# Performance work log

Measured on AMD Instinct MI355X. Metric: run time of the kernel, lower is better.

Reference implementation:

```python
import jax, jax.numpy as jnp
import numpy as np

N_NODES = 100000
N_EDGES = 1000000
NHID = 128
N_CLASSES = 5000


def setup_inputs() -> dict:
    key = jax.random.key(0)
    ks = jax.random.split(key, 8)
    feature = jax.random.normal(ks[0], (N_NODES, NHID), dtype=jnp.float32)
    # Linear weights stored as [in, out] so forward is x @ W + b
    W1 = jax.random.normal(ks[1], (2 * NHID, NHID), dtype=jnp.float32) * (1.0 / np.sqrt(2 * NHID))
    b1 = jnp.zeros((NHID,), dtype=jnp.float32)
    alpha = jnp.full((NHID,), 0.25, dtype=jnp.float32)  # PReLU per-channel init
    W2 = jax.random.normal(ks[2], (NHID, 2), dtype=jnp.float32) * (1.0 / np.sqrt(NHID))
    b2 = jnp.zeros((2,), dtype=jnp.float32)
    row = jax.random.randint(ks[3], (N_EDGES,), 0, N_NODES, dtype=jnp.int64)
    col = jax.random.randint(ks[4], (N_EDGES,), 0, N_NODES, dtype=jnp.int64)
    label = jax.random.randint(ks[5], (N_NODES,), 0, N_CLASSES, dtype=jnp.int64)
    return {"feature": feature, "W1": W1, "b1": b1, "alpha": alpha,
            "W2": W2, "b2": b2, "row": row, "col": col, "label": label}


def reference(feature, W1, b1, alpha, W2, b2, row, col, label):
    # per-edge label: 1 if endpoints share a cluster label
    y = (label[row] == label[col]).astype(jnp.int32)  # [E]
    # edge gather + concat: [E, 2*nhid]
    x = jnp.concatenate([feature[row], feature[col]], axis=1)
    h = x @ W1 + b1                                   # [E, nhid]
    h = jnp.where(h >= 0, h, alpha * h)               # PReLU, per-channel alpha
    logits = h @ W2 + b2                              # [E, 2]
    logp = jax.nn.log_softmax(logits, axis=-1)
    # mean cross-entropy over edges
    loss = -jnp.mean(jnp.take_along_axis(logp, y[:, None], axis=1))
    return loss
```

## Files before the change

kernel.cpp:

```cpp
#include <hip/hip_runtime.h>
#include <hip/hip_bf16.h>

typedef __bf16 bf16_t;
typedef bf16_t bf16x8 __attribute__((ext_vector_type(8)));
typedef float floatx4 __attribute__((ext_vector_type(4)));
typedef float floatx2 __attribute__((ext_vector_type(2)));

#define N_NODES 100000
#define N_EDGES 1000000


__global__ __launch_bounds__(256) void k_prep(const float* __restrict__ W1,
                                              const float* __restrict__ b1,
                                              const float* __restrict__ alpha,
                                              const float* __restrict__ W2,
                                              const float* __restrict__ b2,
                                              bf16_t* __restrict__ WT,
                                              float* __restrict__ wabsp,
                                              float* __restrict__ w1g,
                                              float* __restrict__ constg,
                                              float* __restrict__ out) {
    const int t = threadIdx.x;
    if (blockIdx.x < 128) {
        int i = blockIdx.x * 256 + t;
        int n = i >> 7, k = i & 127;
        float v = (n < 128) ? W1[k * 128 + n] : W1[(k + 128) * 128 + (n - 128)];
        WT[i] = (bf16_t)v;
        return;
    }
    __shared__ float w1L[128];
    if (t < 128) {
        float wd = W2[2 * t + 1] - W2[2 * t];
        float al = alpha[t];
        float w1v = wd * (1.f + al) * 0.5f;
        w1L[t] = w1v;
        w1g[t] = w1v;
        int col = (t & 64) + (t & 3) * 16 + ((t >> 2) & 15);
        float wdc = W2[2 * col + 1] - W2[2 * col];
        wabsp[t] = wdc * (1.f - alpha[col]) * 0.5f;
    }
    __syncthreads();
    if (t < 64) {
        float c = fmaf(w1L[t], b1[t], w1L[t + 64] * b1[t + 64]);
#pragma unroll
        for (int m = 32; m >= 1; m >>= 1) c += __shfl_xor(c, m, 64);
        if (t == 0) { *constg = c + (b2[1] - b2[0]); out[0] = 0.f; }
    }
}

__device__ inline unsigned fp4_code(float x) {
    float a = fabsf(x);
    unsigned code = (unsigned)(a > 0.25f) + (a > 0.75f) + (a > 1.25f) + (a > 1.75f)
                  + (a > 2.5f) + (a > 3.5f) + (a > 5.0f);
    return code | (x < 0.f ? 8u : 0u);
}

__global__ __launch_bounds__(256) void k_gemm(const float* __restrict__ F,
                                              const bf16_t* __restrict__ WT,
                                              const float* __restrict__ b1,
                                              const float* __restrict__ w1g,
                                              const int* __restrict__ label,
                                              unsigned char* __restrict__ PQ4,
                                              float4* __restrict__ aux_g) {
    __shared__ bf16x8 Bs[2048];
    __shared__ float sP1[4][16];
    __shared__ float sP2[4][16];
    const int t = threadIdx.x;
    const int m0 = blockIdx.x * 32;

    const int w = t >> 6, lane = t & 63;
    const int l15 = lane & 15, quad = lane >> 4;
    const int rw = w >> 1, wq = w & 1;

    const int arow = m0 + rw * 16 + l15;
    const float4* Ar = (const float4*)(F + (size_t)arow * 128 + quad * 8);
    float4 fa[4], fb[4];
#pragma unroll
    for (int s = 0; s < 4; ++s) { fa[s] = Ar[s * 8]; fb[s] = Ar[s * 8 + 1]; }

    float w1v[4], bv[4];
#pragma unroll
    for (int nt = 0; nt < 4; ++nt) {
        int c = wq * 64 + nt * 16 + l15;
        w1v[nt] = w1g[c];
        bv[nt] = b1[c];
    }

    const bf16x8* WT8 = (const bf16x8*)WT;
#pragma unroll
    for (int j = 0; j < 8; ++j) {
        int chunk = j * 256 + t;
        int c = chunk >> 4, cc = chunk & 15;
        Bs[c * 16 + (cc ^ (c & 15))] = WT8[chunk];
    }

    bf16x8 Af[4];
#pragma unroll
    for (int s = 0; s < 4; ++s) {
        bf16x8 v;
        v[0] = (bf16_t)fa[s].x; v[1] = (bf16_t)fa[s].y;
        v[2] = (bf16_t)fa[s].z; v[3] = (bf16_t)fa[s].w;
        v[4] = (bf16_t)fb[s].x; v[5] = (bf16_t)fb[s].y;
        v[6] = (bf16_t)fb[s].z; v[7] = (bf16_t)fb[s].w;
        Af[s] = v;
    }
    __syncthreads();

#pragma unroll
    for (int h = 0; h < 2; ++h) {
        floatx4 acc[4] = {};
#pragma unroll
        for (int s = 0; s < 4; ++s) {
            bf16x8 Bf[4];
#pragma unroll
            for (int nt = 0; nt < 4; ++nt) {
                int c = wq * 64 + nt * 16 + l15;
                Bf[nt] = Bs[c * 16 + ((s * 4 + quad) ^ (c & 15))];
            }
#pragma unroll
            for (int nt = 0; nt < 4; ++nt)
                acc[nt] = __builtin_amdgcn_mfma_f32_16x16x32_bf16(Af[s], Bf[nt], acc[nt], 0, 0, 0);
        }

#pragma unroll
        for (int r = 0; r < 4; ++r) {
            float sv = 0.f;
#pragma unroll
            for (int nt = 0; nt < 4; ++nt) sv = fmaf(w1v[nt], acc[nt][r], sv);
#pragma unroll
            for (int m = 8; m >= 1; m >>= 1) sv += __shfl_xor(sv, m, 64);
            if (l15 == 0) {
                if (h == 0) sP1[w][quad * 4 + r] = sv;
                else        sP2[w][quad * 4 + r] = sv;
            }
        }

#pragma unroll
        for (int r = 0; r < 4; ++r) {
            int g = m0 + rw * 16 + quad * 4 + r;
            float v0 = acc[0][r], v1 = acc[1][r], v2 = acc[2][r], v3 = acc[3][r];
            if (h == 0) { v0 += bv[0]; v1 += bv[1]; v2 += bv[2]; v3 += bv[3]; }
            unsigned pk = fp4_code(v0) | (fp4_code(v1) << 4)
                        | (fp4_code(v2) << 8) | (fp4_code(v3) << 12);
            *(unsigned short*)(PQ4 + (size_t)g * 128 + h * 64 + wq * 32 + l15 * 2) =
                (unsigned short)pk;
        }

        if (h == 0) {
            __syncthreads();
#pragma unroll
            for (int j = 0; j < 8; ++j) {
                int chunk = j * 256 + t;
                int c = chunk >> 4, cc = chunk & 15;
                Bs[c * 16 + (cc ^ (c & 15))] = WT8[2048 + chunk];
            }
            __syncthreads();
        }
    }

    __syncthreads();
    if (t < 32) {
        int rw2 = t >> 4, ri = t & 15;
        float s1 = sP1[rw2 * 2][ri] + sP1[rw2 * 2 + 1][ri];
        float s2 = sP2[rw2 * 2][ri] + sP2[rw2 * 2 + 1][ri];
        int g = m0 + rw2 * 16 + ri;
        float4 av = {s1, s2, __int_as_float(label[g]), 0.f};
        aux_g[g] = av;
    }
}

__device__ inline void fp4_decode(unsigned d, unsigned& pe, unsigned& po) {
    unsigned ne = d & 0x0F0F0F0Fu;
    unsigned no = (d >> 4) & 0x0F0F0F0Fu;
    pe = __builtin_amdgcn_perm(0x4C484440u, 0x3C383000u, ne & 0x07070707u)
       | ((ne & 0x08080808u) << 4);
    po = __builtin_amdgcn_perm(0x4C484440u, 0x3C383000u, no & 0x07070707u)
       | ((no & 0x08080808u) << 4);
}

__global__ __launch_bounds__(256) void k_edge_loss(const unsigned char* __restrict__ PQ4,
                                                   const float4* __restrict__ aux,
                                                   const float* __restrict__ wabsp,
                                                   const float* __restrict__ constg,
                                                   const int* __restrict__ row,
                                                   const int* __restrict__ col,
                                                   float* __restrict__ out) {
    const int lg = threadIdx.x & 15;
    const int group = (blockIdx.x * blockDim.x + threadIdx.x) >> 4;
    const int ng = (gridDim.x * blockDim.x) >> 4;

    float wabs[8];
    const float* wb = wabsp + lg * 8;
    wabs[0] = wb[0]; wabs[1] = wb[2]; wabs[2] = wb[4]; wabs[3] = wb[6];
    wabs[4] = wb[1]; wabs[5] = wb[3]; wabs[6] = wb[5]; wabs[7] = wb[7];
    const float CB = *constg;

    float acc = 0.f;
    for (int e = group; e < N_EDGES; e += 8 * ng) {
        int r[8], c[8];
#pragma unroll
        for (int k = 0; k < 8; ++k) {
            int ee = e + k * ng;
            int es = (ee < N_EDGES) ? ee : e;
            r[k] = row[es]; c[k] = col[es];
        }
        unsigned p[8], q[8];
#pragma unroll
        for (int k = 0; k < 8; ++k) {
            p[k] = *(const unsigned*)(PQ4 + (size_t)r[k] * 128 + lg * 4);
            q[k] = *(const unsigned*)(PQ4 + (size_t)c[k] * 128 + 64 + lg * 4);
        }
        int ee2 = e + (lg & 7) * ng;
        int es2 = (ee2 < N_EDGES) ? ee2 : e;
        const int* ibase = (lg < 8) ? row : col;
        float4 a = aux[ibase[es2]];

        float sab[8] = {0.f, 0.f, 0.f, 0.f, 0.f, 0.f, 0.f, 0.f};
#pragma unroll
        for (int k = 0; k < 8; ++k) {
            unsigned pe, po, qe, qo;
            fp4_decode(p[k], pe, po);
            fp4_decode(q[k], qe, qo);
            floatx2 he0 = __builtin_amdgcn_cvt_pk_f32_fp8((int)pe, false)
                        + __builtin_amdgcn_cvt_pk_f32_fp8((int)qe, false);
            floatx2 he1 = __builtin_amdgcn_cvt_pk_f32_fp8((int)pe, true)
                        + __builtin_amdgcn_cvt_pk_f32_fp8((int)qe, true);
            floatx2 ho0 = __builtin_amdgcn_cvt_pk_f32_fp8((int)po, false)
                        + __builtin_amdgcn_cvt_pk_f32_fp8((int)qo, false);
            floatx2 ho1 = __builtin_amdgcn_cvt_pk_f32_fp8((int)po, true)
                        + __builtin_amdgcn_cvt_pk_f32_fp8((int)qo, true);
            float s = sab[k];
            s = fmaf(fabsf(he0[0]), wabs[0], s);
            s = fmaf(fabsf(he0[1]), wabs[1], s);
            s = fmaf(fabsf(he1[0]), wabs[2], s);
            s = fmaf(fabsf(he1[1]), wabs[3], s);
            s = fmaf(fabsf(ho0[0]), wabs[4], s);
            s = fmaf(fabsf(ho0[1]), wabs[5], s);
            s = fmaf(fabsf(ho1[0]), wabs[6], s);
            s = fmaf(fabsf(ho1[1]), wabs[7], s);
            sab[k] = s;
        }
#pragma unroll
        for (int m = 8; m >= 1; m >>= 1) {
#pragma unroll
            for (int k = 0; k < 8; ++k) sab[k] += __shfl_xor(sab[k], m, 16);
        }
        float s2o = __shfl(a.y, (lg + 8) & 15, 16);
        float lzc = __shfl(a.z, (lg + 8) & 15, 16);
        float mysab = sab[0];
#pragma unroll
        for (int k = 1; k < 8; ++k) mysab = (lg == k) ? sab[k] : mysab;
        float D = a.x + s2o + CB + mysab;
        float sgn = (__float_as_int(a.z) == __float_as_int(lzc)) ? -D : D;
        float loss = fmaxf(sgn, 0.f) + __logf(1.f + __expf(-fabsf(sgn)));
        bool vld = (lg < 8) && (e + lg * ng < N_EDGES);
        acc += vld ? loss : 0.f;
    }
#pragma unroll
    for (int m = 32; m >= 1; m >>= 1) acc += __shfl_xor(acc, m, 64);
    __shared__ float sdata[4];
    int lane = threadIdx.x & 63;
    int wv = threadIdx.x >> 6;
    if (lane == 0) sdata[wv] = acc;
    __syncthreads();
    if (threadIdx.x == 0) {
        float s = (sdata[0] + sdata[1]) + (sdata[2] + sdata[3]);
        atomicAdd(out, s * (1.f / (float)N_EDGES));
    }
}

extern "C" void kernel_launch(void* const* d_in, const int* in_sizes, int n_in,
                              void* d_out, int out_size, void* d_ws, size_t ws_size,
                              hipStream_t stream) {
    const float* feature = (const float*)d_in[0];
    const float* W1      = (const float*)d_in[1];
    const float* b1      = (const float*)d_in[2];
    const float* alpha   = (const float*)d_in[3];
    const float* W2      = (const float*)d_in[4];
    const float* b2      = (const float*)d_in[5];
    const int*   row     = (const int*)d_in[6];
    const int*   col     = (const int*)d_in[7];
    const int*   label   = (const int*)d_in[8];
    float* out = (float*)d_out;

    char* ws = (char*)d_ws;
    unsigned char* PQ4 = (unsigned char*)(ws);
    float* aux   = (float*)(ws + 12800000);
    bf16_t* WT   = (bf16_t*)(ws + 14400000);
    float* wabsp = (float*)(ws + 14465536);
    float* w1g   = (float*)(ws + 14466048);
    float* constg= (float*)(ws + 14466560);

    k_prep<<<129, 256, 0, stream>>>(W1, b1, alpha, W2, b2, WT, wabsp, w1g,
                                    constg, out);
    k_gemm<<<3125, 256, 0, stream>>>(feature, WT, b1, w1g, label, PQ4,
                                     (float4*)aux);
    k_edge_loss<<<4096, 256, 0, stream>>>(PQ4, (const float4*)aux, wabsp, constg,
                                          row, col, out);
}
```

Measured before the change: 191.2 us.

## Hardcode two edge batches per thread with all gathers issued upfront and transpose-reduce

The grid-stride loop in the edge-loss kernel is replaced by exactly two 8-edge batches per 16-lane group. The strides are hardcoded to 65536 groups, which assumes a fixed grid size. All index, aux and packed-feature gathers for both batches are issued before any compute, with a sched_barrier, to raise memory-level parallelism. The 8x16 butterfly reduction becomes a transpose-style reduction that halves the number of values at each step, cutting shuffles from 32 to 15. The cost is higher register pressure and the risk of wrong results if the launch grid differs from the assumed size.

```diff
diff --git a/kernel.cpp b/kernel.cpp
--- a/kernel.cpp
+++ b/kernel.cpp
@@ -178,6 +178,62 @@
        | ((no & 0x08080808u) << 4);
 }
 
+__device__ inline float red8x16(float s[8], int lg) {
+#pragma unroll
+    for (int k = 0; k < 8; ++k) s[k] += __shfl_xor(s[k], 8, 16);
+    const bool b4 = (lg & 4) != 0;
+    float u[4];
+#pragma unroll
+    for (int k = 0; k < 4; ++k) {
+        float snd = b4 ? s[k] : s[k + 4];
+        float kp  = b4 ? s[k + 4] : s[k];
+        u[k] = kp + __shfl_xor(snd, 4, 16);
+    }
+    const bool b2 = (lg & 2) != 0;
+    float v[2];
+#pragma unroll
+    for (int k = 0; k < 2; ++k) {
+        float snd = b2 ? u[k] : u[k + 2];
+        float kp  = b2 ? u[k + 2] : u[k];
+        v[k] = kp + __shfl_xor(snd, 2, 16);
+    }
+    const bool b1 = (lg & 1) != 0;
+    float snd = b1 ? v[0] : v[1];
+    float kp  = b1 ? v[1] : v[0];
+    return kp + __shfl_xor(snd, 1, 16);
+}
+
+__device__ inline float edge_batch(const unsigned* __restrict__ p,
+                                   const unsigned* __restrict__ q,
+                                   const float* __restrict__ wabs, int lg) {
+    float sab[8];
+#pragma unroll
+    for (int k = 0; k < 8; ++k) {
+        unsigned pe, po, qe, qo;
+        fp4_decode(p[k], pe, po);
+        fp4_decode(q[k], qe, qo);
+        floatx2 he0 = __builtin_amdgcn_cvt_pk_f32_fp8((int)pe, false)
+                    + __builtin_amdgcn_cvt_pk_f32_fp8((int)qe, false);
+        floatx2 he1 = __builtin_amdgcn_cvt_pk_f32_fp8((int)pe, true)
+                    + __builtin_amdgcn_cvt_pk_f32_fp8((int)qe, true);
+        floatx2 ho0 = __builtin_amdgcn_cvt_pk_f32_fp8((int)po, false)
+                    + __builtin_amdgcn_cvt_pk_f32_fp8((int)qo, false);
+        floatx2 ho1 = __builtin_amdgcn_cvt_pk_f32_fp8((int)po, true)
+                    + __builtin_amdgcn_cvt_pk_f32_fp8((int)qo, true);
+        float s = 0.f;
+        s = fmaf(fabsf(he0[0]), wabs[0], s);
+        s = fmaf(fabsf(he0[1]), wabs[1], s);
+        s = fmaf(fabsf(he1[0]), wabs[2], s);
+        s = fmaf(fabsf(he1[1]), wabs[3], s);
+        s = fmaf(fabsf(ho0[0]), wabs[4], s);
+        s = fmaf(fabsf(ho0[1]), wabs[5], s);
+        s = fmaf(fabsf(ho1[0]), wabs[6], s);
+        s = fmaf(fabsf(ho1[1]), wabs[7], s);
+        sab[k] = s;
+    }
+    return red8x16(sab, lg);
+}
+
 __global__ __launch_bounds__(256) void k_edge_loss(const unsigned char* __restrict__ PQ4,
                                                    const float4* __restrict__ aux,
                                                    const float* __restrict__ wabsp,
@@ -187,75 +243,72 @@
                                                    float* __restrict__ out) {
     const int lg = threadIdx.x & 15;
     const int group = (blockIdx.x * blockDim.x + threadIdx.x) >> 4;
-    const int ng = (gridDim.x * blockDim.x) >> 4;
+    const int e2b = group + 524288;
 
     float wabs[8];
     const float* wb = wabsp + lg * 8;
     wabs[0] = wb[0]; wabs[1] = wb[2]; wabs[2] = wb[4]; wabs[3] = wb[6];
     wabs[4] = wb[1]; wabs[5] = wb[3]; wabs[6] = wb[5]; wabs[7] = wb[7];
     const float CB = *constg;
-
-    float acc = 0.f;
-    for (int e = group; e < N_EDGES; e += 8 * ng) {
-        int r[8], c[8];
-#pragma unroll
-        for (int k = 0; k < 8; ++k) {
-            int ee = e + k * ng;
-            int es = (ee < N_EDGES) ? ee : e;
-            r[k] = row[es]; c[k] = col[es];
-        }
-        unsigned p[8], q[8];
-#pragma unroll
-        for (int k = 0; k < 8; ++k) {
-            p[k] = *(const unsigned*)(PQ4 + (size_t)r[k] * 128 + lg * 4);
-            q[k] = *(const unsigned*)(PQ4 + (size_t)c[k] * 128 + 64 + lg * 4);
-        }
-        int ee2 = e + (lg & 7) * ng;
-        int es2 = (ee2 < N_EDGES) ? ee2 : e;
-        const int* ibase = (lg < 8) ? row : col;
-        float4 a = aux[ibase[es2]];
-
-        float sab[8] = {0.f, 0.f, 0.f, 0.f, 0.f, 0.f, 0.f, 0.f};
-#pragma unroll
-        for (int k = 0; k < 8; ++k) {
-            unsigned pe, po, qe, qo;
-            fp4_decode(p[k], pe, po);
-            fp4_decode(q[k], qe, qo);
-            floatx2 he0 = __builtin_amdgcn_cvt_pk_f32_fp8((int)pe, false)
-                        + __builtin_amdgcn_cvt_pk_f32_fp8((int)qe, false);
-            floatx2 he1 = __builtin_amdgcn_cvt_pk_f32_fp8((int)pe, true)
-                        + __builtin_amdgcn_cvt_pk_f32_fp8((int)qe, true);
-            floatx2 ho0 = __builtin_amdgcn_cvt_pk_f32_fp8((int)po, false)
-                        + __builtin_amdgcn_cvt_pk_f32_fp8((int)qo, false);
-            floatx2 ho1 = __builtin_amdgcn_cvt_pk_f32_fp8((int)po, true)
-                        + __builtin_amdgcn_cvt_pk_f32_fp8((int)qo, true);
-            float s = sab[k];
-            s = fmaf(fabsf(he0[0]), wabs[0], s);
-            s = fmaf(fabsf(he0[1]), wabs[1], s);
-            s = fmaf(fabsf(he1[0]), wabs[2], s);
-            s = fmaf(fabsf(he1[1]), wabs[3], s);
-            s = fmaf(fabsf(ho0[0]), wabs[4], s);
-            s = fmaf(fabsf(ho0[1]), wabs[5], s);
-            s = fmaf(fabsf(ho1[0]), wabs[6], s);
-            s = fmaf(fabsf(ho1[1]), wabs[7], s);
-            sab[k] = s;
-        }
-#pragma unroll
-        for (int m = 8; m >= 1; m >>= 1) {
-#pragma unroll
-            for (int k = 0; k < 8; ++k) sab[k] += __shfl_xor(sab[k], m, 16);
-        }
-        float s2o = __shfl(a.y, (lg + 8) & 15, 16);
-        float lzc = __shfl(a.z, (lg + 8) & 15, 16);
-        float mysab = sab[0];
-#pragma unroll
-        for (int k = 1; k < 8; ++k) mysab = (lg == k) ? sab[k] : mysab;
-        float D = a.x + s2o + CB + mysab;
-        float sgn = (__float_as_int(a.z) == __float_as_int(lzc)) ? -D : D;
+    const unsigned lg4 = (unsigned)lg * 4u;
+
+    const int* ib = (lg < 8) ? row : col;
+    const int a1e = group + (lg & 7) * 65536;
+    const int a2e = e2b + (lg & 7) * 65536;
+    const int a2s = (a2e < N_EDGES) ? a2e : e2b;
+    int ia1 = ib[a1e];
+    int ia2 = ib[a2s];
+
+    int r1[8], c1[8], r2[8], c2[8];
+#pragma unroll
+    for (int k = 0; k < 8; ++k) {
+        int ee = group + k * 65536;
+        r1[k] = row[ee]; c1[k] = col[ee];
+    }
+#pragma unroll
+    for (int k = 0; k < 8; ++k) {
+        int ee = e2b + k * 65536;
+        int es = (k < 7) ? ee : ((ee < N_EDGES) ? ee : e2b);
+        r2[k] = row[es]; c2[k] = col[es];
+    }
+
+    float4 A1 = *(const float4*)((const char*)aux + (unsigned)ia1 * 16u);
+    float4 A2 = *(const float4*)((const char*)aux + (unsigned)ia2 * 16u);
+
+    unsigned p1[8], q1[8], p2[8], q2[8];
+#pragma unroll
+    for (int k = 0; k < 8; ++k) {
+        p1[k] = *(const unsigned*)(PQ4 + ((unsigned)r1[k] * 128u + lg4));
+        q1[k] = *(const unsigned*)(PQ4 + ((unsigned)c1[k] * 128u + 64u + lg4));
+    }
+#pragma unroll
+    for (int k = 0; k < 8; ++k) {
+        p2[k] = *(const unsigned*)(PQ4 + ((unsigned)r2[k] * 128u + lg4));
+        q2[k] = *(const unsigned*)(PQ4 + ((unsigned)c2[k] * 128u + 64u + lg4));
+    }
+    __builtin_amdgcn_sched_barrier(0);
+
+    float T1 = edge_batch(p1, q1, wabs, lg);
+    float acc;
+    {
+        float s2o = __shfl(A1.y, (lg + 8) & 15, 16);
+        float lzc = __shfl(A1.z, (lg + 8) & 15, 16);
+        float D = A1.x + s2o + CB + T1;
+        float sgn = (__float_as_int(A1.z) == __float_as_int(lzc)) ? -D : D;
         float loss = fmaxf(sgn, 0.f) + __logf(1.f + __expf(-fabsf(sgn)));
-        bool vld = (lg < 8) && (e + lg * ng < N_EDGES);
-        acc += vld ? loss : 0.f;
-    }
+        acc = (lg < 8) ? loss : 0.f;
+    }
+
+    float T2 = edge_batch(p2, q2, wabs, lg);
+    {
+        float s2o = __shfl(A2.y, (lg + 8) & 15, 16);
+        float lzc = __shfl(A2.z, (lg + 8) & 15, 16);
+        float D = A2.x + s2o + CB + T2;
+        float sgn = (__float_as_int(A2.z) == __float_as_int(lzc)) ? -D : D;
+        float loss = fmaxf(sgn, 0.f) + __logf(1.f + __expf(-fabsf(sgn)));
+        acc += ((lg < 8) && (a2e < N_EDGES)) ? loss : 0.f;
+    }
+
 #pragma unroll
     for (int m = 32; m >= 1; m >>= 1) acc += __shfl_xor(acc, m, 64);
     __shared__ float sdata[4];
```

After: 191.1 us. Within noise of the previous version (-0.1%).
